# Kernel tuning notes

Measured on AMD Instinct MI355X. Metric: run time of the kernel, lower is better.

## Reference

```python
import jax, jax.numpy as jnp
import numpy as np

N_NODES = 100000
N_EDGES = 3200000
IN_DIM = 62
OUT_DIM = 16
EDGE_DIM = 2


def setup_inputs() -> dict:
    key = jax.random.key(0)
    ks = jax.random.split(key, 8)
    h = jax.random.normal(ks[0], (N_NODES, IN_DIM), dtype=jnp.float32)
    e = jax.random.normal(ks[1], (N_EDGES, EDGE_DIM), dtype=jnp.float32)
    src = jax.random.randint(ks[2], (N_EDGES,), 0, N_NODES, dtype=jnp.int32)
    dst = jax.random.randint(ks[3], (N_EDGES,), 0, N_NODES, dtype=jnp.int32)
    # xavier-normal-ish scaled weights
    W_fc = jax.random.normal(ks[4], (OUT_DIM, IN_DIM), dtype=jnp.float32) * 0.2
    W_attn = jax.random.normal(ks[5], (1, 2 * OUT_DIM + EDGE_DIM), dtype=jnp.float32) * 0.2
    W_edge = jax.random.normal(ks[6], (EDGE_DIM, EDGE_DIM), dtype=jnp.float32) * 0.5
    W_e2n = jax.random.normal(ks[7], (OUT_DIM, EDGE_DIM), dtype=jnp.float32) * 0.5
    return {"h": h, "e": e, "src": src, "dst": dst, "W_fc": W_fc,
            "W_attn": W_attn, "W_edge": W_edge, "W_e2n": W_e2n}


def _agat_forward(h, e, src, dst, W_fc, W_attn, W_edge, W_e2n):
    n = h.shape[0]
    d = W_fc.shape[0]
    z = h @ W_fc.T                      # [N, D]
    ex = e @ W_edge.T                   # [E, edge_dim]
    # attn_fc([z_src, z_dst, ex]) split into per-part projections
    Wa_src = W_attn[:, :d]              # [1, D]
    Wa_dst = W_attn[:, d:2 * d]         # [1, D]
    Wa_e = W_attn[:, 2 * d:]            # [1, edge_dim]
    a_src = (z @ Wa_src.T)[:, 0]        # [N] per-node, gathered per-edge
    a_dst = (z @ Wa_dst.T)[:, 0]        # [N]
    a = a_src[src] + a_dst[dst] + (ex @ Wa_e.T)[:, 0]   # [E]
    e_att = jax.nn.leaky_relu(a, negative_slope=0.01)    # [E]
    # segment softmax over incoming edges of each dst node
    m = jax.ops.segment_max(e_att, dst, num_segments=n)  # [N]
    w = jnp.exp(e_att - m[dst])                           # [E]
    denom = jax.ops.segment_sum(w, dst, num_segments=n)   # [N]
    attn = w / denom[dst]                                  # [E]
    # message = z_src + ez; aggregated as attn-weighted sum (matches
    # sum(attn*z) + sum(attn*ez) in reduce_func)
    ez = ex @ W_e2n.T                                      # [E, D]
    msg = attn[:, None] * (z[src] + ez)                    # [E, D]
    return jax.ops.segment_sum(msg, dst, num_segments=n)   # [N, D]


def reference(h, e, src, dst, W_fc, W_attn, W_edge, W_e2n):
    return _agat_forward(h, e, src, dst, W_fc, W_attn, W_edge, W_e2n)
```

## Files before the change

### kernel.cpp

```cpp
#include <hip/hip_runtime.h>
#include <hip/hip_fp16.h>

#define N_NODES 100000
#define N_EDGES 3200000
#define IN_DIM  62
#define OUT_DIM 16

#define EBC    4096
#define EPT    4
#define NEB    ((N_EDGES + EBC - 1) / EBC)
#define NPB    ((N_NODES + 1023) / 1024)
#define BSH    8
#define BNODES 256
#define NB2    ((N_NODES + BNODES - 1) / BNODES)
#define PCAP   6912
#define CHK    2048
#define CSTR   16
#define PADY   ((int)0x82000000u)

typedef int nat_i2 __attribute__((ext_vector_type(2)));

__global__ __launch_bounds__(1024) void proj_append_kernel(
    const float* __restrict__ h,
    const float* __restrict__ W_fc,
    const float* __restrict__ W_attn,
    const float* __restrict__ e,
    const int*   __restrict__ src,
    const int*   __restrict__ dst,
    __half* __restrict__ zh,
    float* __restrict__ a_src_arr,
    float* __restrict__ a_dst_arr,
    int*   __restrict__ cursor,
    nat_i2* __restrict__ records,
    int cap)
{
    __shared__ int  cnt[NB2];
    __shared__ int  pfx[NB2];
    __shared__ int  combo[NB2];
    __shared__ int2 pay[PCAP];
    __shared__ unsigned short pbkt[PCAP];
    __shared__ int  wsum[16];
    __shared__ int  sh_ptot;

    int tid = threadIdx.x;

    if (blockIdx.x < NPB) {
        int i = blockIdx.x * 1024 + tid;
        if (i >= N_NODES) return;

        float acc[OUT_DIM];
#pragma unroll
        for (int j = 0; j < OUT_DIM; ++j) acc[j] = 0.f;

        const float2* __restrict__ hr = (const float2*)(h + (size_t)i * IN_DIM);
#pragma unroll
        for (int kk = 0; kk < IN_DIM / 2; ++kk) {
            float2 hv = hr[kk];
#pragma unroll
            for (int j = 0; j < OUT_DIM; ++j) {
                acc[j] += hv.x * W_fc[j * IN_DIM + 2 * kk]
                        + hv.y * W_fc[j * IN_DIM + 2 * kk + 1];
            }
        }

        float asrc = 0.f, adst = 0.f;
#pragma unroll
        for (int j = 0; j < OUT_DIM; ++j) {
            asrc += acc[j] * W_attn[j];
            adst += acc[j] * W_attn[OUT_DIM + j];
        }

        union { __half hx[16]; uint4 q[2]; } u;
#pragma unroll
        for (int j = 0; j < OUT_DIM; ++j) u.hx[j] = __float2half(acc[j]);
        uint4* __restrict__ zrow = (uint4*)(zh + (size_t)i * OUT_DIM);
        zrow[0] = u.q[0];
        zrow[1] = u.q[1];

        a_src_arr[i] = asrc;
        a_dst_arr[i] = adst;
        return;
    }

    int be = blockIdx.x - NPB;
    long ebase = (long)be * EBC;
    int chunk_n = (int)min((long)EBC, (long)N_EDGES - ebase);

    int dv[EPT], sv[EPT];
    float2 ev[EPT];
#pragma unroll
    for (int j = 0; j < EPT; ++j) {
        int p = tid + j * 1024;
        dv[j] = -1;
        if (p < chunk_n) {
            long eid = ebase + p;
            dv[j] = dst[eid];
            sv[j] = src[eid];
            ev[j] = ((const float2*)e)[eid];
        }
    }

    for (int t = tid; t < NB2; t += 1024) cnt[t] = 0;
    __syncthreads();

#pragma unroll
    for (int j = 0; j < EPT; ++j)
        if (dv[j] >= 0) atomicAdd(&cnt[dv[j] >> BSH], 1);
    __syncthreads();

    int c = 0, n8 = 0, gb = 0;
    if (tid < NB2) {
        c  = cnt[tid];
        n8 = (c + 7) & ~7;
        cnt[tid] = 0;
        if (n8) gb = atomicAdd(&cursor[tid * CSTR], n8);
    }

    int texcl;
    {
        int lane = tid & 63, wid = tid >> 6;
        int x = n8;
#pragma unroll
        for (int off = 1; off < 64; off <<= 1) {
            int y = __shfl_up(x, off, 64);
            if (lane >= off) x += y;
        }
        if (lane == 63) wsum[wid] = x;
        __syncthreads();
        if (wid == 0) {
            int v = (lane < 16) ? wsum[lane] : 0;
#pragma unroll
            for (int off = 1; off < 16; off <<= 1) {
                int y = __shfl_up(v, off, 64);
                if (lane >= off) v += y;
            }
            if (lane < 16) wsum[lane] = v;
        }
        __syncthreads();
        texcl = x - n8 + (wid ? wsum[wid - 1] : 0);
    }

    if (tid < NB2) {
        pfx[tid]   = texcl;
        combo[tid] = tid * cap + gb - texcl;
        for (int q = texcl; q < texcl + n8; ++q) {
            pay[q]  = make_int2(0, PADY);
            pbkt[q] = (unsigned short)tid;
        }
    }
    if (tid == NB2 - 1) sh_ptot = texcl + n8;
    __syncthreads();

#pragma unroll
    for (int j = 0; j < EPT; ++j) {
        if (dv[j] >= 0) {
            int b = dv[j] >> BSH;
            union { __half2 h2; int i; } uu;
            uu.h2.x = __float2half(ev[j].x);
            uu.h2.y = __float2half(ev[j].y);
            int r = atomicAdd(&cnt[b], 1);
            int q = pfx[b] + r;
            pay[q] = make_int2(uu.i, sv[j] | ((dv[j] & (BNODES - 1)) << 17));
        }
    }
    __syncthreads();

    int ptot = sh_ptot;
    for (int p = tid; p < ptot; p += 1024) {
        int2 v  = pay[p];
        int  bb = pbkt[p];
        int pos = combo[bb] + p;
        if (pos < (bb + 1) * cap) {
            nat_i2 vv; vv.x = v.x; vv.y = v.y;
            __builtin_nontemporal_store(vv, records + pos);
        }
    }
}

__global__ __launch_bounds__(512) void bucket_gather_kernel(
    const int*    __restrict__ cursor,
    const nat_i2* __restrict__ records,
    const __half* __restrict__ zh,
    const float*  __restrict__ a_src_arr,
    const float*  __restrict__ a_dst_arr,
    const float*  __restrict__ W_attn,
    const float*  __restrict__ W_edge,
    const float*  __restrict__ W_e2n,
    float* __restrict__ num,
    float* __restrict__ den,
    int cap)
{
    __shared__ int2 rec[CHK];
    __shared__ unsigned int exb[CHK];
    __shared__ unsigned short inv[CHK];
    __shared__ int hist[257], pfxs[257], cur[257];
    __shared__ float adst_l[BNODES];
    __shared__ int wsum4[4];

    int b   = blockIdx.x >> 1;
    int hb  = blockIdx.x & 1;
    int tid = threadIdx.x;
    long lo = (long)b * cap;
    int n   = cursor[b * CSTR];
    if (n > cap) n = cap;

    if (tid < BNODES) {
        int node = b * BNODES + tid;
        adst_l[tid] = (node < N_NODES) ? a_dst_arr[node] : 0.f;
    }
    __syncthreads();

    float we00 = W_edge[0], we01 = W_edge[1], we10 = W_edge[2], we11 = W_edge[3];
    float wa0  = W_attn[2 * OUT_DIM], wa1 = W_attn[2 * OUT_DIM + 1];

    int lane4 = (tid & 3) * 4;

    float aA[2][4], aW[2], aX0[2], aX1[2];
#pragma unroll
    for (int sp = 0; sp < 2; ++sp) {
        aW[sp] = 0.f; aX0[sp] = 0.f; aX1[sp] = 0.f;
#pragma unroll
        for (int f = 0; f < 4; ++f) aA[sp][f] = 0.f;
    }

    for (int cb = hb * CHK; cb < n; cb += 2 * CHK) {
        int cn = n - cb; if (cn > CHK) cn = CHK;

        __syncthreads();
        if (tid < 257) { hist[tid] = 0; cur[tid] = 0; }
        __syncthreads();

        int ld0 = -1, ld1 = -1, ld2 = -1, ld3 = -1;
#define EDGEW(J, LD)                                                        \
        {                                                                   \
            int kk = tid + (J) * 512;                                       \
            if (kk < cn) {                                                  \
                nat_i2 r = __builtin_nontemporal_load(records + lo + cb + kk); \
                int s = r.y & 0x1FFFF;                                      \
                LD = (r.y >> 17) & 0x1FF;                  \
                union { int i; __half2 h2; } ue; ue.i = r.x;                \
                float e0 = __low2float(ue.h2), e1 = __high2float(ue.h2);    \
                float ex0 = e0 * we00 + e1 * we01;                          \
                float ex1 = e0 * we10 + e1 * we11;                          \
                float a = a_src_arr[s] + adst_l[LD & 255] + ex0 * wa0 + ex1 * wa1; \
                float ea = (a > 0.f) ? a : 0.01f * a;                       \
                float w  = __expf(ea);                                      \
                if (r.y < 0) w = 0.f;                       \
                rec[kk] = make_int2(__float_as_int(w), r.y);                \
                union { unsigned int i; __half2 h2; } up;                   \
                up.h2.x = __float2half(ex0);                                \
                up.h2.y = __float2half(ex1);                                \
                exb[kk] = up.i;                                             \
                atomicAdd(&hist[LD], 1);                                    \
            }                                                               \
        }
        EDGEW(0, ld0) EDGEW(1, ld1) EDGEW(2, ld2) EDGEW(3, ld3)
#undef EDGEW
        __syncthreads();

        int hh = 0, xx = 0;
        int lane = tid & 63, wv = tid >> 6;
        if (tid < 256) {
            hh = hist[tid]; xx = hh;
#pragma unroll
            for (int off = 1; off < 64; off <<= 1) {
                int y = __shfl_up(xx, off, 64);
                if (lane >= off) xx += y;
            }
            if (lane == 63) wsum4[wv] = xx;
        }
        __syncthreads();
        if (tid == 0) {
            int rr = 0;
#pragma unroll
            for (int i2 = 0; i2 < 4; ++i2) { int t = wsum4[i2]; wsum4[i2] = rr; rr += t; }
        }
        __syncthreads();
        if (tid < 256) {
            pfxs[tid] = xx - hh + wsum4[wv];
            if (tid == 255) pfxs[256] = xx + wsum4[3];
        }
        __syncthreads();

#define INVW(J, LD)                                                         \
        if (LD >= 0) {                                                      \
            int kk = tid + (J) * 512;                                       \
            int r = atomicAdd(&cur[LD], 1);                                 \
            inv[pfxs[LD] + r] = (unsigned short)kk;                         \
        }
        INVW(0, ld0) INVW(1, ld1) INVW(2, ld2) INVW(3, ld3)
#undef INVW
        __syncthreads();

#pragma unroll
        for (int sp = 0; sp < 2; ++sp) {
            int nl_  = sp * 128 + (tid >> 2);
            int m    = hist[nl_];
            int base = pfxs[nl_];
            for (int i = 0; i < m; ++i) {
                int k = inv[base + i];
                int2 r = rec[k];
                float w = __int_as_float(r.x);
                int s = r.y & 0x1FFFF;
                unsigned int xe = exb[k];
                uint2 zz = *(const uint2*)(zh + (size_t)s * OUT_DIM + lane4);
                union { unsigned int i; __half2 h2; } za, zb, xu;
                za.i = zz.x; zb.i = zz.y; xu.i = xe;
                aA[sp][0] += w * __low2float(za.h2);
                aA[sp][1] += w * __high2float(za.h2);
                aA[sp][2] += w * __low2float(zb.h2);
                aA[sp][3] += w * __high2float(zb.h2);
                aW[sp]  += w;
                aX0[sp] += w * __low2float(xu.h2);
                aX1[sp] += w * __high2float(xu.h2);
            }
        }
    }

#pragma unroll
    for (int sp = 0; sp < 2; ++sp) {
        int node = b * BNODES + sp * 128 + (tid >> 2);
        if (node < N_NODES) {
#pragma unroll
            for (int f = 0; f < 4; ++f) {
                int j = lane4 + f;
                float ez = aX0[sp] * W_e2n[2 * j] + aX1[sp] * W_e2n[2 * j + 1];
                unsafeAtomicAdd(&num[(size_t)node * OUT_DIM + j], aA[sp][f] + ez);
            }
            if ((tid & 3) == 0) unsafeAtomicAdd(&den[node], aW[sp]);
        }
    }
}

__global__ __launch_bounds__(256) void normalize2_kernel(
    const float* __restrict__ num, const float* __restrict__ den,
    float* __restrict__ out)
{
    int t = blockIdx.x * blockDim.x + threadIdx.x;
    const int total = N_NODES * OUT_DIM / 4;
    if (t >= total) return;
    int node = t >> 2;
    float dn = den[node];
    float iv = (dn != 0.f) ? (1.f / dn) : 0.f;
    float4 v = ((const float4*)num)[t];
    v.x *= iv; v.y *= iv; v.z *= iv; v.w *= iv;
    ((float4*)out)[t] = v;
}


__global__ __launch_bounds__(256) void node_proj_fb_kernel(
    const float* __restrict__ h,
    const float* __restrict__ W_fc,
    const float* __restrict__ W_attn,
    float* __restrict__ z,
    float* __restrict__ a_src_arr,
    float* __restrict__ a_dst_arr,
    float* __restrict__ denom,
    float* __restrict__ out)
{
    int i = blockIdx.x * blockDim.x + threadIdx.x;
    if (i >= N_NODES) return;

    float acc[OUT_DIM];
#pragma unroll
    for (int j = 0; j < OUT_DIM; ++j) acc[j] = 0.f;

    const float2* __restrict__ hr = (const float2*)(h + (size_t)i * IN_DIM);
#pragma unroll
    for (int kk = 0; kk < IN_DIM / 2; ++kk) {
        float2 hv = hr[kk];
#pragma unroll
        for (int j = 0; j < OUT_DIM; ++j) {
            acc[j] += hv.x * W_fc[j * IN_DIM + 2 * kk]
                    + hv.y * W_fc[j * IN_DIM + 2 * kk + 1];
        }
    }

    float asrc = 0.f, adst = 0.f;
#pragma unroll
    for (int j = 0; j < OUT_DIM; ++j) {
        asrc += acc[j] * W_attn[j];
        adst += acc[j] * W_attn[OUT_DIM + j];
    }

    float4* __restrict__ zrow = (float4*)(z + (size_t)i * OUT_DIM);
    zrow[0] = make_float4(acc[0],  acc[1],  acc[2],  acc[3]);
    zrow[1] = make_float4(acc[4],  acc[5],  acc[6],  acc[7]);
    zrow[2] = make_float4(acc[8],  acc[9],  acc[10], acc[11]);
    zrow[3] = make_float4(acc[12], acc[13], acc[14], acc[15]);

    a_src_arr[i] = asrc;
    a_dst_arr[i] = adst;
    denom[i] = 0.f;

    float4 z4 = make_float4(0.f, 0.f, 0.f, 0.f);
    float4* __restrict__ orow = (float4*)(out + (size_t)i * OUT_DIM);
    orow[0] = z4; orow[1] = z4; orow[2] = z4; orow[3] = z4;
}

__global__ __launch_bounds__(256) void edge_kernel(
    const float* __restrict__ e,
    const int*   __restrict__ src,
    const int*   __restrict__ dst,
    const float* __restrict__ W_attn,
    const float* __restrict__ W_edge,
    const float* __restrict__ W_e2n,
    const float* __restrict__ z,
    const float* __restrict__ a_src_arr,
    const float* __restrict__ a_dst_arr,
    float* __restrict__ denom,
    float* __restrict__ out)
{
    int eid = blockIdx.x * blockDim.x + threadIdx.x;
    if (eid >= N_EDGES) return;

    int s = src[eid];
    int d = dst[eid];

    float2 ev = ((const float2*)e)[eid];
    float ex0 = ev.x * W_edge[0] + ev.y * W_edge[1];
    float ex1 = ev.x * W_edge[2] + ev.y * W_edge[3];

    float a = a_src_arr[s] + a_dst_arr[d]
            + ex0 * W_attn[2 * OUT_DIM] + ex1 * W_attn[2 * OUT_DIM + 1];
    float ea = (a > 0.f) ? a : 0.01f * a;
    float w  = __expf(ea);

    unsafeAtomicAdd(denom + d, w);

    const float4* __restrict__ zrow = (const float4*)(z + (size_t)s * OUT_DIM);
    float4 z0 = zrow[0], z1 = zrow[1], z2 = zrow[2], z3 = zrow[3];

    float* __restrict__ orow = out + (size_t)d * OUT_DIM;
    float zs[OUT_DIM] = { z0.x, z0.y, z0.z, z0.w,
                          z1.x, z1.y, z1.z, z1.w,
                          z2.x, z2.y, z2.z, z2.w,
                          z3.x, z3.y, z3.z, z3.w };
#pragma unroll
    for (int j = 0; j < OUT_DIM; ++j) {
        float ez = ex0 * W_e2n[2 * j] + ex1 * W_e2n[2 * j + 1];
        unsafeAtomicAdd(orow + j, w * (zs[j] + ez));
    }
}

__global__ __launch_bounds__(256) void normalize_kernel(
    float* __restrict__ out, const float* __restrict__ denom)
{
    int tid = blockIdx.x * blockDim.x + threadIdx.x;
    const int total = N_NODES * OUT_DIM / 4;
    if (tid >= total) return;
    int n = tid >> 2;
    float dn = denom[n];
    float inv = (dn != 0.f) ? (1.f / dn) : 0.f;
    float4 v = ((float4*)out)[tid];
    v.x *= inv; v.y *= inv; v.z *= inv; v.w *= inv;
    ((float4*)out)[tid] = v;
}

extern "C" void kernel_launch(void* const* d_in, const int* in_sizes, int n_in,
                              void* d_out, int out_size, void* d_ws, size_t ws_size,
                              hipStream_t stream)
{
    const float* h      = (const float*)d_in[0];
    const float* e      = (const float*)d_in[1];
    const int*   src    = (const int*)  d_in[2];
    const int*   dst    = (const int*)  d_in[3];
    const float* W_fc   = (const float*)d_in[4];
    const float* W_attn = (const float*)d_in[5];
    const float* W_edge = (const float*)d_in[6];
    const float* W_e2n  = (const float*)d_in[7];
    float* out = (float*)d_out;

    char* ws = (char*)d_ws;

    size_t off = 0;
    __half* zh        = (__half*)(ws + off); off += (size_t)N_NODES * OUT_DIM * 2;
    float*  a_src_arr = (float*) (ws + off); off += (size_t)N_NODES * 4;
    float*  a_dst_arr = (float*) (ws + off); off += (size_t)N_NODES * 4;
    off = (off + 255) & ~(size_t)255;
    size_t mz_off = off;
    int*    cursor = (int*)(ws + off);  off += ((size_t)NB2 * CSTR * 4 + 255) & ~(size_t)255;
    float*  num    = (float*)(ws + off); off += (size_t)N_NODES * OUT_DIM * 4;
    float*  den    = (float*)(ws + off); off += (size_t)N_NODES * 4;
    size_t mz_bytes = off - mz_off;
    size_t rec_off = (off + 255) & ~(size_t)255;

    int cap = 0;
    if      (ws_size >= rec_off + (size_t)NB2 * 12288 * 8) cap = 12288;
    else if (ws_size >= rec_off + (size_t)NB2 * 11776 * 8) cap = 11776;

    if (cap) {
        nat_i2* records = (nat_i2*)(ws + rec_off);

        hipMemsetAsync(ws + mz_off, 0, mz_bytes, stream);

        proj_append_kernel<<<NPB + NEB, 1024, 0, stream>>>(
            h, W_fc, W_attn, e, src, dst,
            zh, a_src_arr, a_dst_arr, cursor, records, cap);

        bucket_gather_kernel<<<2 * NB2, 512, 0, stream>>>(
            cursor, records, zh, a_src_arr, a_dst_arr,
            W_attn, W_edge, W_e2n, num, den, cap);

        normalize2_kernel<<<(N_NODES * OUT_DIM / 4 + 255) / 256, 256, 0, stream>>>(
            num, den, out);
    } else {
        size_t foff = 0;
        float* z     = (float*)(ws + foff); foff += (size_t)N_NODES * OUT_DIM * 4;
        float* asrc  = (float*)(ws + foff); foff += (size_t)N_NODES * 4;
        float* adst  = (float*)(ws + foff); foff += (size_t)N_NODES * 4;
        float* denom = (float*)(ws + foff); foff += (size_t)N_NODES * 4;

        node_proj_fb_kernel<<<(N_NODES + 255) / 256, 256, 0, stream>>>(
            h, W_fc, W_attn, z, asrc, adst, denom, out);

        edge_kernel<<<(N_EDGES + 255) / 256, 256, 0, stream>>>(
            e, src, dst, W_attn, W_edge, W_e2n, z, asrc, adst, denom, out);

        normalize_kernel<<<(N_NODES * OUT_DIM / 4 + 255) / 256, 256, 0, stream>>>(
            out, denom);
    }
}
```

Before: 234.1 us.

## Accumulate per-bucket aggregates in LDS atomics and fuse normalization into gather

The gather kernel drops the per-chunk histogram, prefix-scan and inverse-index sort. Each edge now atomically adds its weighted message, weight and edge terms into a per-node shared-memory accumulator, and one 1024-thread block owns a whole bucket. With a single block per bucket the global num/den atomics, their memset and the separate normalize kernel go away, and the output is written directly. The cost is many LDS float atomics per edge (19 per edge), with contention on hot nodes, and less parallelism per bucket. The append kernel also changes how padding slots and bucket ids are written.

```diff
diff --git a/kernel.cpp b/kernel.cpp
--- a/kernel.cpp
+++ b/kernel.cpp
@@ -13,10 +13,10 @@
 #define BSH    8
 #define BNODES 256
 #define NB2    ((N_NODES + BNODES - 1) / BNODES)
-#define PCAP   6912
-#define CHK    2048
+#define PCAP   6840
 #define CSTR   16
 #define PADY   ((int)0x82000000u)
+#define ACCS   21
 
 typedef int nat_i2 __attribute__((ext_vector_type(2)));
 
@@ -143,7 +143,7 @@
     if (tid < NB2) {
         pfx[tid]   = texcl;
         combo[tid] = tid * cap + gb - texcl;
-        for (int q = texcl; q < texcl + n8; ++q) {
+        for (int q = texcl + c; q < texcl + n8; ++q) {
             pay[q]  = make_int2(0, PADY);
             pbkt[q] = (unsigned short)tid;
         }
@@ -160,7 +160,8 @@
             uu.h2.y = __float2half(ev[j].y);
             int r = atomicAdd(&cnt[b], 1);
             int q = pfx[b] + r;
-            pay[q] = make_int2(uu.i, sv[j] | ((dv[j] & (BNODES - 1)) << 17));
+            pay[q]  = make_int2(uu.i, sv[j] | ((dv[j] & (BNODES - 1)) << 17));
+            pbkt[q] = (unsigned short)b;
         }
     }
     __syncthreads();
@@ -177,7 +178,7 @@
     }
 }
 
-__global__ __launch_bounds__(512) void bucket_gather_kernel(
+__global__ __launch_bounds__(1024) void bucket_gather_kernel(
     const int*    __restrict__ cursor,
     const nat_i2* __restrict__ records,
     const __half* __restrict__ zh,
@@ -186,165 +187,83 @@
     const float*  __restrict__ W_attn,
     const float*  __restrict__ W_edge,
     const float*  __restrict__ W_e2n,
-    float* __restrict__ num,
-    float* __restrict__ den,
-    int cap)
-{
-    __shared__ int2 rec[CHK];
-    __shared__ unsigned int exb[CHK];
-    __shared__ unsigned short inv[CHK];
-    __shared__ int hist[257], pfxs[257], cur[257];
+    float* __restrict__ out, int cap)
+{
+    __shared__ float acc[BNODES * ACCS];
     __shared__ float adst_l[BNODES];
-    __shared__ int wsum4[4];
-
-    int b   = blockIdx.x >> 1;
-    int hb  = blockIdx.x & 1;
+    __shared__ float we2n[2 * OUT_DIM];
+
+    int b   = blockIdx.x;
     int tid = threadIdx.x;
     long lo = (long)b * cap;
     int n   = cursor[b * CSTR];
     if (n > cap) n = cap;
 
+    for (int t = tid; t < BNODES * ACCS; t += 1024) acc[t] = 0.f;
     if (tid < BNODES) {
         int node = b * BNODES + tid;
         adst_l[tid] = (node < N_NODES) ? a_dst_arr[node] : 0.f;
     }
+    if (tid < 2 * OUT_DIM) we2n[tid] = W_e2n[tid];
     __syncthreads();
 
     float we00 = W_edge[0], we01 = W_edge[1], we10 = W_edge[2], we11 = W_edge[3];
     float wa0  = W_attn[2 * OUT_DIM], wa1 = W_attn[2 * OUT_DIM + 1];
 
-    int lane4 = (tid & 3) * 4;
-
-    float aA[2][4], aW[2], aX0[2], aX1[2];
-#pragma unroll
-    for (int sp = 0; sp < 2; ++sp) {
-        aW[sp] = 0.f; aX0[sp] = 0.f; aX1[sp] = 0.f;
-#pragma unroll
-        for (int f = 0; f < 4; ++f) aA[sp][f] = 0.f;
-    }
-
-    for (int cb = hb * CHK; cb < n; cb += 2 * CHK) {
-        int cn = n - cb; if (cn > CHK) cn = CHK;
-
-        __syncthreads();
-        if (tid < 257) { hist[tid] = 0; cur[tid] = 0; }
-        __syncthreads();
-
-        int ld0 = -1, ld1 = -1, ld2 = -1, ld3 = -1;
-#define EDGEW(J, LD)                                                        \
-        {                                                                   \
-            int kk = tid + (J) * 512;                                       \
-            if (kk < cn) {                                                  \
-                nat_i2 r = __builtin_nontemporal_load(records + lo + cb + kk); \
-                int s = r.y & 0x1FFFF;                                      \
-                LD = (r.y >> 17) & 0x1FF;                  \
-                union { int i; __half2 h2; } ue; ue.i = r.x;                \
-                float e0 = __low2float(ue.h2), e1 = __high2float(ue.h2);    \
-                float ex0 = e0 * we00 + e1 * we01;                          \
-                float ex1 = e0 * we10 + e1 * we11;                          \
-                float a = a_src_arr[s] + adst_l[LD & 255] + ex0 * wa0 + ex1 * wa1; \
-                float ea = (a > 0.f) ? a : 0.01f * a;                       \
-                float w  = __expf(ea);                                      \
-                if (r.y < 0) w = 0.f;                       \
-                rec[kk] = make_int2(__float_as_int(w), r.y);                \
-                union { unsigned int i; __half2 h2; } up;                   \
-                up.h2.x = __float2half(ex0);                                \
-                up.h2.y = __float2half(ex1);                                \
-                exb[kk] = up.i;                                             \
-                atomicAdd(&hist[LD], 1);                                    \
-            }                                                               \
-        }
-        EDGEW(0, ld0) EDGEW(1, ld1) EDGEW(2, ld2) EDGEW(3, ld3)
-#undef EDGEW
-        __syncthreads();
-
-        int hh = 0, xx = 0;
-        int lane = tid & 63, wv = tid >> 6;
-        if (tid < 256) {
-            hh = hist[tid]; xx = hh;
-#pragma unroll
-            for (int off = 1; off < 64; off <<= 1) {
-                int y = __shfl_up(xx, off, 64);
-                if (lane >= off) xx += y;
-            }
-            if (lane == 63) wsum4[wv] = xx;
-        }
-        __syncthreads();
-        if (tid == 0) {
-            int rr = 0;
-#pragma unroll
-            for (int i2 = 0; i2 < 4; ++i2) { int t = wsum4[i2]; wsum4[i2] = rr; rr += t; }
-        }
-        __syncthreads();
-        if (tid < 256) {
-            pfxs[tid] = xx - hh + wsum4[wv];
-            if (tid == 255) pfxs[256] = xx + wsum4[3];
-        }
-        __syncthreads();
-
-#define INVW(J, LD)                                                         \
-        if (LD >= 0) {                                                      \
-            int kk = tid + (J) * 512;                                       \
-            int r = atomicAdd(&cur[LD], 1);                                 \
-            inv[pfxs[LD] + r] = (unsigned short)kk;                         \
-        }
-        INVW(0, ld0) INVW(1, ld1) INVW(2, ld2) INVW(3, ld3)
-#undef INVW
-        __syncthreads();
-
-#pragma unroll
-        for (int sp = 0; sp < 2; ++sp) {
-            int nl_  = sp * 128 + (tid >> 2);
-            int m    = hist[nl_];
-            int base = pfxs[nl_];
-            for (int i = 0; i < m; ++i) {
-                int k = inv[base + i];
-                int2 r = rec[k];
-                float w = __int_as_float(r.x);
-                int s = r.y & 0x1FFFF;
-                unsigned int xe = exb[k];
-                uint2 zz = *(const uint2*)(zh + (size_t)s * OUT_DIM + lane4);
-                union { unsigned int i; __half2 h2; } za, zb, xu;
-                za.i = zz.x; zb.i = zz.y; xu.i = xe;
-                aA[sp][0] += w * __low2float(za.h2);
-                aA[sp][1] += w * __high2float(za.h2);
-                aA[sp][2] += w * __low2float(zb.h2);
-                aA[sp][3] += w * __high2float(zb.h2);
-                aW[sp]  += w;
-                aX0[sp] += w * __low2float(xu.h2);
-                aX1[sp] += w * __high2float(xu.h2);
-            }
-        }
-    }
-
-#pragma unroll
-    for (int sp = 0; sp < 2; ++sp) {
-        int node = b * BNODES + sp * 128 + (tid >> 2);
+    for (int p = tid; p < n; p += 1024) {
+        nat_i2 r = __builtin_nontemporal_load(records + lo + p);
+        if (r.y < 0) continue;
+        int s  = r.y & 0x1FFFF;
+        int ld = (r.y >> 17) & 255;
+
+        union { int i; __half2 h2; } ue; ue.i = r.x;
+        float e0 = __low2float(ue.h2), e1 = __high2float(ue.h2);
+        float ex0 = e0 * we00 + e1 * we01;
+        float ex1 = e0 * we10 + e1 * we11;
+        float a  = a_src_arr[s] + adst_l[ld] + ex0 * wa0 + ex1 * wa1;
+        float ea = (a > 0.f) ? a : 0.01f * a;
+        float w  = __expf(ea);
+
+        const uint4* __restrict__ zr = (const uint4*)(zh + (size_t)s * OUT_DIM);
+        uint4 z0 = zr[0], z1 = zr[1];
+        float* ab = acc + ld * ACCS;
+        union { unsigned int u; __half2 h2; } t2;
+        t2.u = z0.x; atomicAdd(ab + 0,  w * __low2float(t2.h2));
+                     atomicAdd(ab + 1,  w * __high2float(t2.h2));
+        t2.u = z0.y; atomicAdd(ab + 2,  w * __low2float(t2.h2));
+                     atomicAdd(ab + 3,  w * __high2float(t2.h2));
+        t2.u = z0.z; atomicAdd(ab + 4,  w * __low2float(t2.h2));
+                     atomicAdd(ab + 5,  w * __high2float(t2.h2));
+        t2.u = z0.w; atomicAdd(ab + 6,  w * __low2float(t2.h2));
+                     atomicAdd(ab + 7,  w * __high2float(t2.h2));
+        t2.u = z1.x; atomicAdd(ab + 8,  w * __low2float(t2.h2));
+                     atomicAdd(ab + 9,  w * __high2float(t2.h2));
+        t2.u = z1.y; atomicAdd(ab + 10, w * __low2float(t2.h2));
+                     atomicAdd(ab + 11, w * __high2float(t2.h2));
+        t2.u = z1.z; atomicAdd(ab + 12, w * __low2float(t2.h2));
+                     atomicAdd(ab + 13, w * __high2float(t2.h2));
+        t2.u = z1.w; atomicAdd(ab + 14, w * __low2float(t2.h2));
+                     atomicAdd(ab + 15, w * __high2float(t2.h2));
+        atomicAdd(ab + 16, w);
+        atomicAdd(ab + 17, w * ex0);
+        atomicAdd(ab + 18, w * ex1);
+    }
+    __syncthreads();
+
+#pragma unroll
+    for (int rp = 0; rp < 4; ++rp) {
+        int idx  = rp * 1024 + tid;
+        int ln   = idx >> 4;
+        int j    = idx & 15;
+        int node = b * BNODES + ln;
         if (node < N_NODES) {
-#pragma unroll
-            for (int f = 0; f < 4; ++f) {
-                int j = lane4 + f;
-                float ez = aX0[sp] * W_e2n[2 * j] + aX1[sp] * W_e2n[2 * j + 1];
-                unsafeAtomicAdd(&num[(size_t)node * OUT_DIM + j], aA[sp][f] + ez);
-            }
-            if ((tid & 3) == 0) unsafeAtomicAdd(&den[node], aW[sp]);
-        }
-    }
-}
-
-__global__ __launch_bounds__(256) void normalize2_kernel(
-    const float* __restrict__ num, const float* __restrict__ den,
-    float* __restrict__ out)
-{
-    int t = blockIdx.x * blockDim.x + threadIdx.x;
-    const int total = N_NODES * OUT_DIM / 4;
-    if (t >= total) return;
-    int node = t >> 2;
-    float dn = den[node];
-    float iv = (dn != 0.f) ? (1.f / dn) : 0.f;
-    float4 v = ((const float4*)num)[t];
-    v.x *= iv; v.y *= iv; v.z *= iv; v.w *= iv;
-    ((float4*)out)[t] = v;
+            const float* ab = acc + ln * ACCS;
+            float accw = ab[16];
+            float ez   = ab[17] * we2n[2 * j] + ab[18] * we2n[2 * j + 1];
+            float iv   = (accw != 0.f) ? (1.f / accw) : 0.f;
+            out[(size_t)node * OUT_DIM + j] = (ab[j] + ez) * iv;
+        }
+    }
 }
 
 
@@ -478,11 +397,9 @@
     float*  a_src_arr = (float*) (ws + off); off += (size_t)N_NODES * 4;
     float*  a_dst_arr = (float*) (ws + off); off += (size_t)N_NODES * 4;
     off = (off + 255) & ~(size_t)255;
-    size_t mz_off = off;
-    int*    cursor = (int*)(ws + off);  off += ((size_t)NB2 * CSTR * 4 + 255) & ~(size_t)255;
-    float*  num    = (float*)(ws + off); off += (size_t)N_NODES * OUT_DIM * 4;
-    float*  den    = (float*)(ws + off); off += (size_t)N_NODES * 4;
-    size_t mz_bytes = off - mz_off;
+    int*    cursor = (int*)(ws + off);
+    size_t  cur_bytes = (size_t)NB2 * CSTR * 4;
+    off += (cur_bytes + 255) & ~(size_t)255;
     size_t rec_off = (off + 255) & ~(size_t)255;
 
     int cap = 0;
@@ -492,18 +409,15 @@
     if (cap) {
         nat_i2* records = (nat_i2*)(ws + rec_off);
 
-        hipMemsetAsync(ws + mz_off, 0, mz_bytes, stream);
+        hipMemsetAsync(cursor, 0, cur_bytes, stream);
 
         proj_append_kernel<<<NPB + NEB, 1024, 0, stream>>>(
             h, W_fc, W_attn, e, src, dst,
             zh, a_src_arr, a_dst_arr, cursor, records, cap);
 
-        bucket_gather_kernel<<<2 * NB2, 512, 0, stream>>>(
+        bucket_gather_kernel<<<NB2, 1024, 0, stream>>>(
             cursor, records, zh, a_src_arr, a_dst_arr,
-            W_attn, W_edge, W_e2n, num, den, cap);
-
-        normalize2_kernel<<<(N_NODES * OUT_DIM / 4 + 255) / 256, 256, 0, stream>>>(
-            num, den, out);
+            W_attn, W_edge, W_e2n, out, cap);
     } else {
         size_t foff = 0;
         float* z     = (float*)(ws + foff); foff += (size_t)N_NODES * OUT_DIM * 4;
```

New measurement: 539.8 us. 2.31x slower.
